# Optimization experiments

Measured on AMD Instinct MI355X. Metric: run time of the kernel, lower is better.

Reference implementation:

```python
import jax, jax.numpy as jnp
import numpy as np

B, QL, D = 4, 1024, 1024
H, HD = 16, 64
KVL = 2048


def setup_inputs() -> dict:
    key = jax.random.key(0)
    ks = jax.random.split(key, 6)
    scale = 1.0 / np.sqrt(D)
    return {
        "hidden_states": jax.random.normal(ks[0], (B, QL, D), dtype=jnp.float32),
        "key_states": jax.random.normal(ks[1], (B, H, KVL, HD), dtype=jnp.float32),
        "value_states": jax.random.normal(ks[2], (B, H, KVL, HD), dtype=jnp.float32),
        "attention_mask": jnp.zeros((B, 1, 1, KVL), dtype=jnp.float32),
        "Wq": jax.random.normal(ks[3], (D, D), dtype=jnp.float32) * scale,
        "Wo": jax.random.normal(ks[4], (D, D), dtype=jnp.float32) * scale,
    }


def reference(hidden_states, key_states, value_states, attention_mask, Wq, Wo):
    batch = hidden_states.shape[0]
    # Q projection (T5 Linear has no bias), split heads: [B, H, Q, HD]
    q = jnp.einsum("bqd,de->bqe", hidden_states, Wq)
    q = q.reshape(batch, -1, H, HD).transpose(0, 2, 1, 3)
    # NOTE: T5 attention has NO 1/sqrt(d) scaling
    scores = jnp.einsum("bhqd,bhkd->bhqk", q, key_states) + attention_mask
    attn = jax.nn.softmax(scores.astype(jnp.float32), axis=-1).astype(scores.dtype)
    out = jnp.einsum("bhqk,bhkd->bhqd", attn, value_states)
    out = out.transpose(0, 2, 1, 3).reshape(batch, -1, H * HD)
    return jnp.einsum("bqe,ed->bqd", out, Wo)
```

## Files before the change

kernel.cpp:

```cpp
#include <hip/hip_runtime.h>
#include <hip/hip_bf16.h>
#include <hip/hip_fp16.h>
#include <stdint.h>

typedef _Float16 f16;
typedef _Float16 f16x4 __attribute__((ext_vector_type(4)));
typedef _Float16 f16x8 __attribute__((ext_vector_type(8)));
typedef float f32x4 __attribute__((ext_vector_type(4)));
typedef float f32x16 __attribute__((ext_vector_type(16)));

#define B_ 4
#define QL_ 1024
#define D_ 1024
#define H_ 16
#define HD_ 64
#define KVL_ 2048
#define L2E 1.44269504088896f

__device__ __forceinline__ void g2lds16(const void* g, void* l) {
    __builtin_amdgcn_global_load_lds(
        (const __attribute__((address_space(1))) uint32_t*)g,
        (__attribute__((address_space(3))) uint32_t*)l,
        16, 0, 0);
}

union U8 { uint32_t u[4]; f16x8 v; };

__device__ __forceinline__ uint32_t pkrtz(float a, float b) {
    auto t = __builtin_amdgcn_cvt_pkrtz(a, b);
    return __builtin_bit_cast(uint32_t, t);
}

__global__ void cvt_both(const float* __restrict__ a, f16* __restrict__ da, int n4a,
                         const float* __restrict__ b, f16* __restrict__ db, int n4b) {
    int i = blockIdx.x * blockDim.x + threadIdx.x;
    int st = gridDim.x * blockDim.x;
    int tot = n4a + n4b;
    for (; i < tot; i += st) {
        float4 v = (i < n4a) ? ((const float4*)a)[i] : ((const float4*)b)[i - n4a];
        f16x4 o = { (f16)v.x, (f16)v.y, (f16)v.z, (f16)v.w };
        if (i < n4a) ((f16x4*)da)[i] = o; else ((f16x4*)db)[i - n4a] = o;
    }
}

__global__ void wt_transpose2(const float* __restrict__ s0, f16* __restrict__ d0p,
                              const float* __restrict__ s1, f16* __restrict__ d1p) {
    __shared__ float t[64][65];
    const float* src = blockIdx.x < 256 ? s0 : s1;
    f16* dst = blockIdx.x < 256 ? d0p : d1p;
    int bid = blockIdx.x & 255;
    int k0 = (bid >> 4) << 6;
    int n0 = (bid & 15) << 6;
    int tid = threadIdx.x;
    int rr = tid >> 4;
    int c4 = (tid & 15) << 2;
#pragma unroll
    for (int i = 0; i < 4; ++i) {
        int r = i * 16 + rr;
        float4 v = *(const float4*)(src + (size_t)(k0 + r) * 1024 + n0 + c4);
        t[r][c4 + 0] = v.x; t[r][c4 + 1] = v.y; t[r][c4 + 2] = v.z; t[r][c4 + 3] = v.w;
    }
    __syncthreads();
#pragma unroll
    for (int i = 0; i < 4; ++i) {
        int n = i * 16 + rr;
        f16x4 o;
#pragma unroll
        for (int j = 0; j < 4; ++j) o[j] = (f16)t[c4 + j][n];
        *(f16x4*)(dst + (size_t)(n0 + n) * 1024 + k0 + c4) = o;
    }
}

__global__ void v_transpose(const float* __restrict__ src, f16* __restrict__ dst) {
    __shared__ float t[64][65];
    int bh = blockIdx.x >> 5;
    int kv0 = (blockIdx.x & 31) << 6;
    int tid = threadIdx.x;
    int rr = tid >> 4;
    int c4 = (tid & 15) << 2;
    const int permq[4] = {0, 2, 1, 3};
    int pc4 = (c4 & ~15) + permq[(c4 >> 2) & 3] * 4;
#pragma unroll
    for (int i = 0; i < 4; ++i) {
        int r = i * 16 + rr;
        float4 v = *(const float4*)(src + ((size_t)bh * KVL_ + kv0 + r) * HD_ + c4);
        t[r][c4 + 0] = v.x; t[r][c4 + 1] = v.y; t[r][c4 + 2] = v.z; t[r][c4 + 3] = v.w;
    }
    __syncthreads();
#pragma unroll
    for (int i = 0; i < 4; ++i) {
        int d = i * 16 + rr;
        f16x4 o;
#pragma unroll
        for (int j = 0; j < 4; ++j) o[j] = (f16)t[c4 + j][d];
        *(f16x4*)(dst + ((size_t)bh * HD_ + d) * KVL_ + kv0 + pc4) = o;
    }
}

template <int EPI>
__global__ __launch_bounds__(512) void gemm_tn(
    const f16* __restrict__ A, const f16* __restrict__ BT, void* __restrict__ Cout,
    int M, int N, int K) {
    __shared__ char Alds[2][16384];
    __shared__ char Blds[2][8192];
    int d0 = blockIdx.x;
    int xcd = d0 & 7, sx = d0 >> 3;
    int bm = xcd * 4 + (sx & 3);
    int bn = sx >> 2;
    int tid = threadIdx.x, w = tid >> 6, l = tid & 63;
    int l15 = l & 15, lg = l >> 4;
    int wm = w >> 1, wn = w & 1;
    f32x4 acc[2][2] = {};

    const char* ag[2]; int ao[2];
#pragma unroll
    for (int jj = 0; jj < 2; ++jj) {
        int instr = w + 8 * jj;
        int r = instr * 8 + (l >> 3);
        int cc = (l & 7) ^ (r & 7);
        ag[jj] = (const char*)A + ((size_t)(bm * 128 + r) * K + cc * 8) * 2;
        ao[jj] = instr * 1024;
    }
    int rB = w * 8 + (l >> 3);
    int ccB = (l & 7) ^ (rB & 7);
    const char* bgp = (const char*)BT + ((size_t)(bn * 64 + rB) * K + ccB * 8) * 2;
    int boB = w * 1024;

#define GSTAGE(buf, kt)                                       \
    {                                                         \
        g2lds16(ag[0] + (size_t)(kt) * 128, &Alds[buf][ao[0]]); \
        g2lds16(ag[1] + (size_t)(kt) * 128, &Alds[buf][ao[1]]); \
        g2lds16(bgp + (size_t)(kt) * 128, &Blds[buf][boB]);     \
    }

    int nk = K >> 6;
    GSTAGE(0, 0);
    asm volatile("s_waitcnt vmcnt(0)" ::: "memory");
    __syncthreads();

    for (int kt = 0; kt < nk; ++kt) {
        int cur = kt & 1;
        if (kt + 1 < nk) GSTAGE(cur ^ 1, kt + 1);
#pragma unroll
        for (int ks = 0; ks < 2; ++ks) {
            f16x8 af[2], bf[2];
#pragma unroll
            for (int m = 0; m < 2; ++m) {
                int r = wm * 32 + m * 16 + l15;
                af[m] = *(const f16x8*)(&Alds[cur][r * 128 + ((ks * 64 + lg * 16) ^ ((r & 7) << 4))]);
            }
#pragma unroll
            for (int n = 0; n < 2; ++n) {
                int r = wn * 32 + n * 16 + l15;
                bf[n] = *(const f16x8*)(&Blds[cur][r * 128 + ((ks * 64 + lg * 16) ^ ((r & 7) << 4))]);
            }
#pragma unroll
            for (int m = 0; m < 2; ++m)
#pragma unroll
                for (int n = 0; n < 2; ++n)
                    acc[m][n] = __builtin_amdgcn_mfma_f32_16x16x32_f16(af[m], bf[n], acc[m][n], 0, 0, 0);
        }
        asm volatile("s_waitcnt vmcnt(0)" ::: "memory");
        __syncthreads();
    }

#pragma unroll
    for (int m = 0; m < 2; ++m)
#pragma unroll
        for (int n = 0; n < 2; ++n)
#pragma unroll
            for (int i = 0; i < 4; ++i) {
                int row = bm * 128 + wm * 32 + m * 16 + lg * 4 + i;
                int col = bn * 64 + wn * 32 + n * 16 + l15;
                if (EPI == 0) {
                    float v = acc[m][n][i] * L2E;
                    int b = row >> 10, q = row & 1023, h = col >> 6, d = col & 63;
                    ((f16*)Cout)[(((size_t)b * H_ + h) * QL_ + q) * HD_ + d] = (f16)v;
                } else {
                    ((float*)Cout)[(size_t)row * N + col] = acc[m][n][i];
                }
            }
#undef GSTAGE
}

__global__ __launch_bounds__(512, 4) void attn_fused(
    const f16* __restrict__ qh, const f16* __restrict__ kh, const f16* __restrict__ vt,
    const float* __restrict__ mask, f16* __restrict__ aout) {
    __shared__ char lds_buf[65536];
    __shared__ float frl[8][32];
    __shared__ float fr2[4][2][32];
    __shared__ float2 msx[4][32];

    int tid = threadIdx.x, w = tid >> 6, l = tid & 63;
    int l31 = l & 31, hi = l >> 5;
    int swl = (l31 & 7) << 4;
    int g = w >> 2, wg = w & 3;
    int d0 = blockIdx.x;
    int xcd = d0 & 7, sx = d0 >> 3;
    int bh = xcd * 8 + (sx & 7);
    int qt = sx >> 3;
    int b = bh >> 4, h = bh & 15;

    char* Kst = lds_buf + g * 32768;
    char* Vst = lds_buf + g * 32768 + 16384;

    f16x8 Qf[4];
    {
        const f16* qp = qh + ((size_t)bh * QL_ + qt * 128 + wg * 32 + l31) * HD_ + hi * 8;
#pragma unroll
        for (int ds_ = 0; ds_ < 4; ++ds_) Qf[ds_] = *(const f16x8*)(qp + ds_ * 16);
    }

    const char* kg0; const char* vg0; int ko0, vo0;
    {
        int instr = wg;
        int r = instr * 8 + (l >> 3);
        int cc = (l & 7) ^ (r & 7);
        kg0 = (const char*)kh + ((size_t)bh * KVL_ + g * 1024 + r) * 128 + cc * 16;
        ko0 = instr * 1024;
        vg0 = (const char*)vt + ((size_t)bh * HD_ + r) * (KVL_ * 2) + g * 2048 + cc * 16;
        vo0 = instr * 1024;
    }

#define ASTAGE(buf, ch)                                                              \
    {                                                                                \
        g2lds16(kg0 + (size_t)(ch) * 8192, Kst + (buf) * 8192 + ko0);                \
        g2lds16(kg0 + (size_t)(ch) * 8192 + 4096, Kst + (buf) * 8192 + ko0 + 4096);  \
        g2lds16(vg0 + (size_t)(ch) * 128, Vst + (buf) * 8192 + vo0);                 \
        g2lds16(vg0 + (size_t)(ch) * 128 + 131072, Vst + (buf) * 8192 + vo0 + 4096); \
    }

    float mrun = -1e30f, ssum = 0.f;
    f32x16 acc[2] = {};
    const float* mpb = mask + b * KVL_ + g * 1024;

    ASTAGE(0, 0);
    asm volatile("s_waitcnt vmcnt(0)" ::: "memory");
    __syncthreads();

    for (int ch = 0; ch < 16; ++ch) {
        int cur = ch & 1;
        if (ch + 1 < 16) ASTAGE(cur ^ 1, ch + 1);
        const char* Kc = Kst + cur * 8192;
        const char* Vc = Vst + cur * 8192;

#pragma unroll
        for (int kb = 0; kb < 2; ++kb) {
            f32x16 St = {};
            __builtin_amdgcn_s_setprio(1);
#pragma unroll
            for (int ds_ = 0; ds_ < 4; ++ds_) {
                f16x8 kf = *(const f16x8*)(Kc + (kb * 32 + l31) * 128 + ((ds_ * 32 + hi * 16) ^ swl));
                St = __builtin_amdgcn_mfma_f32_32x32x16_f16(kf, Qf[ds_], St, 0, 0, 0);
            }
            __builtin_amdgcn_s_setprio(0);
#pragma unroll
            for (int g4 = 0; g4 < 4; ++g4) {
                f32x4 mv = *(const f32x4*)(mpb + ch * 64 + kb * 32 + g4 * 8 + hi * 4);
#pragma unroll
                for (int j = 0; j < 4; ++j) St[g4 * 4 + j] += mv[j] * L2E;
            }

            float q0 = fmaxf(fmaxf(St[0], St[1]), fmaxf(St[2], St[3]));
            float q1 = fmaxf(fmaxf(St[4], St[5]), fmaxf(St[6], St[7]));
            float q2 = fmaxf(fmaxf(St[8], St[9]), fmaxf(St[10], St[11]));
            float q3 = fmaxf(fmaxf(St[12], St[13]), fmaxf(St[14], St[15]));
            float pm = fmaxf(fmaxf(q0, q1), fmaxf(q2, q3));
            pm = fmaxf(pm, __shfl_xor(pm, 32));

            if (__any(pm > mrun + 12.f)) {
                float mn = fmaxf(mrun, pm);
                float fac = exp2f(mrun - mn);
                mrun = mn;
                ssum *= fac;
                frl[w][l31] = fac;
                asm volatile("s_waitcnt lgkmcnt(0)" ::: "memory");
#pragma unroll
                for (int g4 = 0; g4 < 4; ++g4) {
                    f32x4 fv = *(const f32x4*)&frl[w][g4 * 8 + hi * 4];
#pragma unroll
                    for (int c = 0; c < 2; ++c)
#pragma unroll
                        for (int j = 0; j < 4; ++j) acc[c][g4 * 4 + j] *= fv[j];
                }
            }

#pragma unroll
            for (int r = 0; r < 16; ++r) {
                float p = exp2f(St[r] - mrun);
                St[r] = p;
                ssum += p;
            }

            __builtin_amdgcn_s_setprio(1);
#pragma unroll
            for (int sti = 0; sti < 2; ++sti) {
                U8 pa;
                int half = sti * 8;
#pragma unroll
                for (int ii = 0; ii < 4; ++ii)
                    pa.u[ii] = pkrtz(St[half + 2 * ii], St[half + 2 * ii + 1]);
                int st_ = kb * 2 + sti;
#pragma unroll
                for (int c = 0; c < 2; ++c) {
                    U8 vb;
                    vb.v = *(const f16x8*)(Vc + (c * 32 + l31) * 128 + ((st_ * 32 + hi * 16) ^ swl));
                    acc[c] = __builtin_amdgcn_mfma_f32_32x32x16_f16(pa.v, vb.v, acc[c], 0, 0, 0);
                }
            }
            __builtin_amdgcn_s_setprio(0);
        }
        asm volatile("s_waitcnt vmcnt(0)" ::: "memory");
        __syncthreads();
    }

    ssum += __shfl_xor(ssum, 32);
    char* exch = lds_buf;
    if (g == 1) {
        int base = (wg * 64 + l) * 128;
#pragma unroll
        for (int i = 0; i < 8; ++i) {
            int c = i >> 2, j0 = (i & 3) * 4;
            f32x4 vv = { acc[c][j0], acc[c][j0 + 1], acc[c][j0 + 2], acc[c][j0 + 3] };
            *(f32x4*)(exch + base + ((i * 16) ^ ((l & 7) << 4))) = vv;
        }
        if (hi == 0) msx[wg][l31] = make_float2(mrun, ssum);
    }
    __syncthreads();
    if (g == 0) {
        float2 mb = msx[wg][l31];
        float m = fmaxf(mrun, mb.x);
        float fA = exp2f(mrun - m), fB = exp2f(mb.x - m);
        float s = ssum * fA + mb.y * fB;
        float rinv = 1.0f / s;
        if (hi == 0) { fr2[wg][0][l31] = fA * rinv; fr2[wg][1][l31] = fB * rinv; }
        asm volatile("s_waitcnt lgkmcnt(0)" ::: "memory");
        int base = (wg * 64 + l) * 128;
#pragma unroll
        for (int c = 0; c < 2; ++c)
#pragma unroll
            for (int g4 = 0; g4 < 4; ++g4) {
                f32x4 gAv = *(const f32x4*)&fr2[wg][0][g4 * 8 + hi * 4];
                f32x4 gBv = *(const f32x4*)&fr2[wg][1][g4 * 8 + hi * 4];
                int i = c * 4 + g4;
                f32x4 pv = *(const f32x4*)(exch + base + ((i * 16) ^ ((l & 7) << 4)));
#pragma unroll
                for (int j = 0; j < 4; ++j) {
                    float o = acc[c][g4 * 4 + j] * gAv[j] + pv[j] * gBv[j];
                    int q = qt * 128 + wg * 32 + g4 * 8 + hi * 4 + j;
                    int dd = c * 32 + l31;
                    aout[((size_t)b * QL_ + q) * D_ + h * HD_ + dd] = (f16)o;
                }
            }
    }
#undef ASTAGE
}

extern "C" void kernel_launch(void* const* d_in, const int* in_sizes, int n_in,
                              void* d_out, int out_size, void* d_ws, size_t ws_size,
                              hipStream_t stream) {
    const float* hs = (const float*)d_in[0];
    const float* K  = (const float*)d_in[1];
    const float* V  = (const float*)d_in[2];
    const float* mask = (const float*)d_in[3];
    const float* Wq = (const float*)d_in[4];
    const float* Wo = (const float*)d_in[5];
    float* out = (float*)d_out;
    char* ws = (char*)d_ws;

    f16* hs_h = (f16*)(ws + 0);
    f16* Wq_t = (f16*)(ws + 8388608);
    f16* Wo_t = (f16*)(ws + 10485760);
    f16* K_h  = (f16*)(ws + 12582912);
    f16* V_t  = (f16*)(ws + 29360128);
    f16* q_h  = (f16*)(ws + 46137344);
    f16* a_o  = (f16*)(ws + 54525952);

    cvt_both<<<2048, 256, 0, stream>>>(hs, hs_h, (B_ * QL_ * D_) / 4,
                                       K, K_h, (B_ * H_ * KVL_ * HD_) / 4);
    wt_transpose2<<<512, 256, 0, stream>>>(Wq, Wq_t, Wo, Wo_t);
    v_transpose<<<2048, 256, 0, stream>>>(V, V_t);

    gemm_tn<0><<<512, 512, 0, stream>>>(hs_h, Wq_t, (void*)q_h, 4096, 1024, 1024);
    attn_fused<<<512, 512, 0, stream>>>(q_h, K_h, V_t, mask, a_o);
    gemm_tn<1><<<512, 512, 0, stream>>>(a_o, Wo_t, (void*)out, 4096, 1024, 1024);
}
```

Before: 123.1 us.

## Merge preprocessing kernels, prescale mask, and fuse softmax sum into packed dot

Merges the three preprocessing launches into one kernel that also writes a mask prescaled by log2(e). The attention loop now seeds the QK^T accumulator with the mask instead of adding it after the MFMAs. The exp results are packed to fp16 once, and the row sum is accumulated with fdot2 on the packed values, which removes separate adds and duplicate conversions. The risk is small precision drift, because the sum is now taken over fp16-rounded probabilities.

```diff
diff --git a/kernel.cpp b/kernel.cpp
--- a/kernel.cpp
+++ b/kernel.cpp
@@ -4,6 +4,7 @@
 #include <stdint.h>
 
 typedef _Float16 f16;
+typedef _Float16 f16x2 __attribute__((ext_vector_type(2)));
 typedef _Float16 f16x4 __attribute__((ext_vector_type(4)));
 typedef _Float16 f16x8 __attribute__((ext_vector_type(8)));
 typedef float f32x4 __attribute__((ext_vector_type(4)));
@@ -31,69 +32,74 @@
     return __builtin_bit_cast(uint32_t, t);
 }
 
-__global__ void cvt_both(const float* __restrict__ a, f16* __restrict__ da, int n4a,
-                         const float* __restrict__ b, f16* __restrict__ db, int n4b) {
-    int i = blockIdx.x * blockDim.x + threadIdx.x;
-    int st = gridDim.x * blockDim.x;
-    int tot = n4a + n4b;
-    for (; i < tot; i += st) {
-        float4 v = (i < n4a) ? ((const float4*)a)[i] : ((const float4*)b)[i - n4a];
-        f16x4 o = { (f16)v.x, (f16)v.y, (f16)v.z, (f16)v.w };
-        if (i < n4a) ((f16x4*)da)[i] = o; else ((f16x4*)db)[i - n4a] = o;
-    }
-}
-
-__global__ void wt_transpose2(const float* __restrict__ s0, f16* __restrict__ d0p,
-                              const float* __restrict__ s1, f16* __restrict__ d1p) {
+__global__ void preprocess(const float* __restrict__ hs, f16* __restrict__ hs_h,
+                           const float* __restrict__ K, f16* __restrict__ K_h,
+                           const float* __restrict__ Wq, f16* __restrict__ Wq_t,
+                           const float* __restrict__ Wo, f16* __restrict__ Wo_t,
+                           const float* __restrict__ V, f16* __restrict__ V_t,
+                           const float* __restrict__ mask, float* __restrict__ mL) {
     __shared__ float t[64][65];
-    const float* src = blockIdx.x < 256 ? s0 : s1;
-    f16* dst = blockIdx.x < 256 ? d0p : d1p;
-    int bid = blockIdx.x & 255;
-    int k0 = (bid >> 4) << 6;
-    int n0 = (bid & 15) << 6;
-    int tid = threadIdx.x;
-    int rr = tid >> 4;
-    int c4 = (tid & 15) << 2;
-#pragma unroll
-    for (int i = 0; i < 4; ++i) {
-        int r = i * 16 + rr;
-        float4 v = *(const float4*)(src + (size_t)(k0 + r) * 1024 + n0 + c4);
-        t[r][c4 + 0] = v.x; t[r][c4 + 1] = v.y; t[r][c4 + 2] = v.z; t[r][c4 + 3] = v.w;
-    }
-    __syncthreads();
-#pragma unroll
-    for (int i = 0; i < 4; ++i) {
-        int n = i * 16 + rr;
-        f16x4 o;
-#pragma unroll
-        for (int j = 0; j < 4; ++j) o[j] = (f16)t[c4 + j][n];
-        *(f16x4*)(dst + (size_t)(n0 + n) * 1024 + k0 + c4) = o;
-    }
-}
-
-__global__ void v_transpose(const float* __restrict__ src, f16* __restrict__ dst) {
-    __shared__ float t[64][65];
-    int bh = blockIdx.x >> 5;
-    int kv0 = (blockIdx.x & 31) << 6;
-    int tid = threadIdx.x;
-    int rr = tid >> 4;
-    int c4 = (tid & 15) << 2;
-    const int permq[4] = {0, 2, 1, 3};
-    int pc4 = (c4 & ~15) + permq[(c4 >> 2) & 3] * 4;
-#pragma unroll
-    for (int i = 0; i < 4; ++i) {
-        int r = i * 16 + rr;
-        float4 v = *(const float4*)(src + ((size_t)bh * KVL_ + kv0 + r) * HD_ + c4);
-        t[r][c4 + 0] = v.x; t[r][c4 + 1] = v.y; t[r][c4 + 2] = v.z; t[r][c4 + 3] = v.w;
-    }
-    __syncthreads();
-#pragma unroll
-    for (int i = 0; i < 4; ++i) {
-        int d = i * 16 + rr;
-        f16x4 o;
-#pragma unroll
-        for (int j = 0; j < 4; ++j) o[j] = (f16)t[c4 + j][d];
-        *(f16x4*)(dst + ((size_t)bh * HD_ + d) * KVL_ + kv0 + pc4) = o;
+    int bid = blockIdx.x, tid = threadIdx.x;
+    if (bid < 2048) {
+        const int n4a = (B_ * QL_ * D_) / 4;
+        const int n4b = (B_ * H_ * KVL_ * HD_) / 4;
+        int i = bid * 256 + tid;
+        int st = 2048 * 256;
+        for (; i < n4a + n4b; i += st) {
+            float4 v = (i < n4a) ? ((const float4*)hs)[i] : ((const float4*)K)[i - n4a];
+            f16x4 o = { (f16)v.x, (f16)v.y, (f16)v.z, (f16)v.w };
+            if (i < n4a) ((f16x4*)hs_h)[i] = o; else ((f16x4*)K_h)[i - n4a] = o;
+        }
+    } else if (bid < 2560) {
+        int wbid = bid - 2048;
+        const float* src = wbid < 256 ? Wq : Wo;
+        f16* dst = wbid < 256 ? Wq_t : Wo_t;
+        int b2 = wbid & 255;
+        int k0 = (b2 >> 4) << 6, n0 = (b2 & 15) << 6;
+        int rr = tid >> 4, c4 = (tid & 15) << 2;
+#pragma unroll
+        for (int i = 0; i < 4; ++i) {
+            int r = i * 16 + rr;
+            float4 v = *(const float4*)(src + (size_t)(k0 + r) * 1024 + n0 + c4);
+            t[r][c4 + 0] = v.x; t[r][c4 + 1] = v.y; t[r][c4 + 2] = v.z; t[r][c4 + 3] = v.w;
+        }
+        __syncthreads();
+#pragma unroll
+        for (int i = 0; i < 4; ++i) {
+            int n = i * 16 + rr;
+            f16x4 o;
+#pragma unroll
+            for (int j = 0; j < 4; ++j) o[j] = (f16)t[c4 + j][n];
+            *(f16x4*)(dst + (size_t)(n0 + n) * 1024 + k0 + c4) = o;
+        }
+    } else if (bid < 4608) {
+        int vbid = bid - 2560;
+        int bh = vbid >> 5, kv0 = (vbid & 31) << 6;
+        int rr = tid >> 4, c4 = (tid & 15) << 2;
+        const int permq[4] = {0, 2, 1, 3};
+        int pc4 = (c4 & ~15) + permq[(c4 >> 2) & 3] * 4;
+#pragma unroll
+        for (int i = 0; i < 4; ++i) {
+            int r = i * 16 + rr;
+            float4 v = *(const float4*)(V + ((size_t)bh * KVL_ + kv0 + r) * HD_ + c4);
+            t[r][c4 + 0] = v.x; t[r][c4 + 1] = v.y; t[r][c4 + 2] = v.z; t[r][c4 + 3] = v.w;
+        }
+        __syncthreads();
+#pragma unroll
+        for (int i = 0; i < 4; ++i) {
+            int d = i * 16 + rr;
+            f16x4 o;
+#pragma unroll
+            for (int j = 0; j < 4; ++j) o[j] = (f16)t[c4 + j][d];
+            *(f16x4*)(V_t + ((size_t)bh * HD_ + d) * KVL_ + kv0 + pc4) = o;
+        }
+    } else {
+        int i = (bid - 4608) * 256 + tid;
+        if (i < (B_ * KVL_) / 4) {
+            f32x4 v = ((const f32x4*)mask)[i];
+            v *= L2E;
+            ((f32x4*)mL)[i] = v;
+        }
     }
 }
 
@@ -185,7 +191,7 @@
 
 __global__ __launch_bounds__(512, 4) void attn_fused(
     const f16* __restrict__ qh, const f16* __restrict__ kh, const f16* __restrict__ vt,
-    const float* __restrict__ mask, f16* __restrict__ aout) {
+    const float* __restrict__ mL, f16* __restrict__ aout) {
     __shared__ char lds_buf[65536];
     __shared__ float frl[8][32];
     __shared__ float fr2[4][2][32];
@@ -232,7 +238,8 @@
 
     float mrun = -1e30f, ssum = 0.f;
     f32x16 acc[2] = {};
-    const float* mpb = mask + b * KVL_ + g * 1024;
+    const float* mpb = mL + b * KVL_ + g * 1024;
+    const f16x2 one2 = { (f16)1.0f, (f16)1.0f };
 
     ASTAGE(0, 0);
     asm volatile("s_waitcnt vmcnt(0)" ::: "memory");
@@ -246,7 +253,13 @@
 
 #pragma unroll
         for (int kb = 0; kb < 2; ++kb) {
-            f32x16 St = {};
+            f32x16 St;
+#pragma unroll
+            for (int g4 = 0; g4 < 4; ++g4) {
+                f32x4 mv = *(const f32x4*)(mpb + ch * 64 + kb * 32 + g4 * 8 + hi * 4);
+                St[g4 * 4 + 0] = mv[0]; St[g4 * 4 + 1] = mv[1];
+                St[g4 * 4 + 2] = mv[2]; St[g4 * 4 + 3] = mv[3];
+            }
             __builtin_amdgcn_s_setprio(1);
 #pragma unroll
             for (int ds_ = 0; ds_ < 4; ++ds_) {
@@ -254,18 +267,13 @@
                 St = __builtin_amdgcn_mfma_f32_32x32x16_f16(kf, Qf[ds_], St, 0, 0, 0);
             }
             __builtin_amdgcn_s_setprio(0);
-#pragma unroll
-            for (int g4 = 0; g4 < 4; ++g4) {
-                f32x4 mv = *(const f32x4*)(mpb + ch * 64 + kb * 32 + g4 * 8 + hi * 4);
-#pragma unroll
-                for (int j = 0; j < 4; ++j) St[g4 * 4 + j] += mv[j] * L2E;
-            }
-
-            float q0 = fmaxf(fmaxf(St[0], St[1]), fmaxf(St[2], St[3]));
-            float q1 = fmaxf(fmaxf(St[4], St[5]), fmaxf(St[6], St[7]));
-            float q2 = fmaxf(fmaxf(St[8], St[9]), fmaxf(St[10], St[11]));
-            float q3 = fmaxf(fmaxf(St[12], St[13]), fmaxf(St[14], St[15]));
-            float pm = fmaxf(fmaxf(q0, q1), fmaxf(q2, q3));
+
+            float a0 = fmaxf(fmaxf(St[0], St[1]), St[2]);
+            float a1 = fmaxf(fmaxf(St[3], St[4]), St[5]);
+            float a2 = fmaxf(fmaxf(St[6], St[7]), St[8]);
+            float a3 = fmaxf(fmaxf(St[9], St[10]), St[11]);
+            float a4 = fmaxf(fmaxf(St[12], St[13]), St[14]);
+            float pm = fmaxf(fmaxf(fmaxf(a0, a1), St[15]), fmaxf(fmaxf(a2, a3), a4));
             pm = fmaxf(pm, __shfl_xor(pm, 32));
 
             if (__any(pm > mrun + 12.f)) {
@@ -285,21 +293,22 @@
                 }
             }
 
-#pragma unroll
-            for (int r = 0; r < 16; ++r) {
-                float p = exp2f(St[r] - mrun);
-                St[r] = p;
-                ssum += p;
+            uint32_t pk[8];
+#pragma unroll
+            for (int i = 0; i < 8; ++i) {
+                float p0 = exp2f(St[2 * i] - mrun);
+                float p1 = exp2f(St[2 * i + 1] - mrun);
+                uint32_t u = pkrtz(p0, p1);
+                pk[i] = u;
+                ssum = __builtin_amdgcn_fdot2(__builtin_bit_cast(f16x2, u), one2, ssum, false);
             }
 
             __builtin_amdgcn_s_setprio(1);
 #pragma unroll
             for (int sti = 0; sti < 2; ++sti) {
                 U8 pa;
-                int half = sti * 8;
-#pragma unroll
-                for (int ii = 0; ii < 4; ++ii)
-                    pa.u[ii] = pkrtz(St[half + 2 * ii], St[half + 2 * ii + 1]);
+                pa.u[0] = pk[sti * 4 + 0]; pa.u[1] = pk[sti * 4 + 1];
+                pa.u[2] = pk[sti * 4 + 2]; pa.u[3] = pk[sti * 4 + 3];
                 int st_ = kb * 2 + sti;
 #pragma unroll
                 for (int c = 0; c < 2; ++c) {
@@ -375,13 +384,11 @@
     f16* V_t  = (f16*)(ws + 29360128);
     f16* q_h  = (f16*)(ws + 46137344);
     f16* a_o  = (f16*)(ws + 54525952);
-
-    cvt_both<<<2048, 256, 0, stream>>>(hs, hs_h, (B_ * QL_ * D_) / 4,
-                                       K, K_h, (B_ * H_ * KVL_ * HD_) / 4);
-    wt_transpose2<<<512, 256, 0, stream>>>(Wq, Wq_t, Wo, Wo_t);
-    v_transpose<<<2048, 256, 0, stream>>>(V, V_t);
-
+    float* mL = (float*)(ws + 62914560);
+
+    preprocess<<<4616, 256, 0, stream>>>(hs, hs_h, K, K_h, Wq, Wq_t, Wo, Wo_t,
+                                         V, V_t, mask, mL);
     gemm_tn<0><<<512, 512, 0, stream>>>(hs_h, Wq_t, (void*)q_h, 4096, 1024, 1024);
-    attn_fused<<<512, 512, 0, stream>>>(q_h, K_h, V_t, mask, a_o);
+    attn_fused<<<512, 512, 0, stream>>>(q_h, K_h, V_t, mL, a_o);
     gemm_tn<1><<<512, 512, 0, stream>>>(a_o, Wo_t, (void*)out, 4096, 1024, 1024);
 }
```

New measurement: 117.6 us. 1.05x faster.
